# Kernel tuning notes

Measured on AMD Instinct MI355X. Metric: run time of the kernel, lower is better.

## Reference

```python
import jax, jax.numpy as jnp
import numpy as np

N = 4096      # num_nodes
D = 16        # intrinsic embed_dim (manifold points live in R^{D+1})
H = 64        # NCA hidden_dim
K_CURV = 1.0  # curvature K
SQRT_K = 1.0
TAU = 0.5     # temperature (distance decay)
K0 = 1.0      # coupling_strength
DT_PHASE = 0.1
DT_NCA = 0.1
EPS = 1e-7


def mdot(u, v):
    # Minkowski inner product <u,v>_L = -u0*v0 + sum_i ui*vi
    return jnp.sum(u[..., 1:] * v[..., 1:], axis=-1) - u[..., 0] * v[..., 0]


def proj_tangent(x, v):
    # project v onto tangent space at x: v + K<x,v>_L x
    return v + K_CURV * mdot(x, v)[..., None] * x


def exp_map(x, v):
    n = jnp.sqrt(jnp.clip(mdot(v, v), EPS))[..., None]
    return jnp.cosh(SQRT_K * n) * x + jnp.sinh(SQRT_K * n) / (SQRT_K * n) * v


def setup_inputs() -> dict:
    key = jax.random.key(0)
    ks = jax.random.split(key, 6)
    adjacency = jax.random.uniform(ks[0], (N, N), dtype=jnp.float32)
    # stable_initialization: tangent vector of radius 0.5, exp-mapped from origin
    v = jax.random.normal(ks[1], (N, D), dtype=jnp.float32)
    v = v * 0.5 / (jnp.linalg.norm(v, axis=-1, keepdims=True) + 1e-8)
    v_full = jnp.concatenate([jnp.zeros((N, 1), jnp.float32), v], axis=-1)
    origin = jnp.concatenate(
        [jnp.full((N, 1), 1.0 / SQRT_K, jnp.float32), jnp.zeros((N, D), jnp.float32)], axis=-1)
    h_states = exp_map(origin, proj_tangent(origin, v_full))
    # HAKORN Kuramoto parameters: per-node phases and natural frequencies
    theta = jax.random.uniform(ks[2], (N,), dtype=jnp.float32, minval=0.0, maxval=2.0 * np.pi)
    omega = jax.random.normal(ks[3], (N,), dtype=jnp.float32) * 0.1
    # NCA MLP weights (tangent-space update network)
    W1 = jax.random.normal(ks[4], (D + 1, H), jnp.float32) / np.sqrt(D + 1)
    b1 = jnp.zeros((H,), jnp.float32)
    W2 = jax.random.normal(ks[5], (H, D + 1), jnp.float32) / np.sqrt(H)
    b2 = jnp.zeros((D + 1,), jnp.float32)
    return {"adjacency": adjacency, "h_states": h_states, "theta": theta,
            "omega": omega, "W1": W1, "b1": b1, "W2": W2, "b2": b2, "num_steps": 2}


def _step(h, adjacency, theta, omega, W1, b1, W2, b2):
    X = h  # [N, D+1]
    # pairwise Minkowski gram G_ij = <x_i, x_j>_L  [N, N]
    G = X[:, 1:] @ X[:, 1:].T - jnp.outer(X[:, 0], X[:, 0])
    # hyperbolic distance matrix
    dmat = jnp.arccosh(jnp.clip(-K_CURV * G, 1.0)) / SQRT_K
    # distance-decayed adjacency coupling
    C = adjacency * jnp.exp(-dmat / TAU)
    # --- h_akorn: Kuramoto phase coupling (one Euler step), matvec form ---
    cs, sn = jnp.cos(theta), jnp.sin(theta)
    dtheta = omega + (K0 / N) * (cs * (C @ sn) - sn * (C @ cs))
    th = theta + DT_PHASE * dtheta
    cs2, sn2 = jnp.cos(th), jnp.sin(th)
    # phase-gated modulation weights [N, N]
    M = C * (0.5 * (1.0 + jnp.outer(cs2, cs2) + jnp.outer(sn2, sn2)))
    # synchronization order parameter r = |mean e^{i th}|
    r = jnp.sqrt(jnp.mean(cs2) ** 2 + jnp.mean(sn2) ** 2)
    # --- h_nca: weighted log-map aggregation + MLP + exp-map update ---
    # log_{x_i}(x_j) = alpha_ij * (x_j + K G_ij x_i),
    # alpha_ij = d_ij / ||x_j + K G_ij x_i||_L = d_ij / sqrt(K G_ij^2 - 1/K)
    unorm = jnp.sqrt(jnp.clip(K_CURV * G * G - 1.0 / K_CURV, EPS))
    alpha = jnp.where(dmat > 1e-6, dmat / unorm, 0.0)
    B = M * alpha  # [N, N]
    # m_i = sum_j B_ij x_j + K x_i sum_j B_ij G_ij  (avoids [N,N,D+1] tensor)
    m = B @ X + K_CURV * jnp.sum(B * G, axis=1, keepdims=True) * X
    v = jnp.tanh(m @ W1 + b1) @ W2 + b2
    v = proj_tangent(X, v)
    h_new = exp_map(X, DT_NCA * v)
    return h_new, M, r


def reference(adjacency, h_states, theta, omega, W1, b1, W2, b2, num_steps):
    h = h_states
    M = jnp.zeros_like(adjacency)
    r = jnp.asarray(0.0, h.dtype)
    for _ in range(num_steps):
        h, M, r = _step(h, adjacency, theta, omega, W1, b1, W2, b2)
    return h, M, r
```

## Files before the change

### kernel.cpp

```cpp
#include <hip/hip_runtime.h>
#include <math.h>

#define NN  4096
#define DP1 17
#define HID 64
#define EPSF 1e-7f

__device__ __forceinline__ float frcp(float x)  { return __builtin_amdgcn_rcpf(x); }
__device__ __forceinline__ float fsqrt(float x) { return __builtin_amdgcn_sqrtf(x); }
__device__ __forceinline__ float flogn(float x) { return __builtin_amdgcn_logf(x) * 0.69314718055994531f; }

__device__ __forceinline__ float uload(const float* __restrict__ p) {
    return __int_as_float(__builtin_amdgcn_readfirstlane(__float_as_int(*p)));
}

__device__ __forceinline__ float wred(float v) {
#pragma unroll
    for (int o = 32; o > 0; o >>= 1) v += __shfl_down(v, o, 64);
    return v;
}

__global__ __launch_bounds__(256) void initk(const float* __restrict__ h0,
                                             const float* __restrict__ theta,
                                             float* __restrict__ xt,
                                             float* __restrict__ snth,
                                             float* __restrict__ csth,
                                             float* __restrict__ racc) {
    int idx = blockIdx.x * 256 + threadIdx.x;
    if (idx < NN * DP1) {
        int i = idx / DP1, k = idx % DP1;
        xt[k * NN + i] = h0[idx];
    }
    if (idx < NN) {
        float t = theta[idx];
        snth[idx] = sinf(t);
        csth[idx] = cosf(t);
    }
    if (idx < 4) racc[idx] = 0.0f;
}

template <int R>
__global__ __launch_bounds__(256) void phaseA(const float* __restrict__ adj,
                                              const float* __restrict__ xrm,
                                              const float* __restrict__ xt,
                                              const float* __restrict__ snth,
                                              const float* __restrict__ csth,
                                              float* __restrict__ sumsn,
                                              float* __restrict__ sumcs) {
    const int tid = threadIdx.x;
    const int row0 = blockIdx.x * R;

    float xi[R][DP1];
#pragma unroll
    for (int r = 0; r < R; ++r)
#pragma unroll
        for (int k = 0; k < DP1; ++k) xi[r][k] = uload(xrm + (row0 + r) * DP1 + k);

    float accs[R], accc[R];
#pragma unroll
    for (int r = 0; r < R; ++r) { accs[r] = 0.f; accc[r] = 0.f; }

    for (int c = tid; c < NN; c += 256) {
        float xj[DP1];
#pragma unroll
        for (int k = 0; k < DP1; ++k) xj[k] = xt[k * NN + c];
        const float snj = snth[c], csj = csth[c];
#pragma unroll
        for (int r = 0; r < R; ++r) {
            float g = -xi[r][0] * xj[0];
#pragma unroll
            for (int k = 1; k < DP1; ++k) g = fmaf(xi[r][k], xj[k], g);
            const float a = fmaxf(-g, 1.0f);
            const float s = fsqrt(fmaxf(fmaf(a, a, -1.0f), 0.0f));
            const float t = a + s;
            const float e = frcp(t * t);
            const float Cij = adj[(row0 + r) * NN + c] * e;
            accs[r] = fmaf(Cij, snj, accs[r]);
            accc[r] = fmaf(Cij, csj, accc[r]);
        }
    }

    __shared__ float red[2 * R][4];
    const int wid = tid >> 6, lane = tid & 63;
#pragma unroll
    for (int r = 0; r < R; ++r) {
        float v1 = wred(accs[r]);
        float v2 = wred(accc[r]);
        if (lane == 0) { red[2 * r][wid] = v1; red[2 * r + 1][wid] = v2; }
    }
    __syncthreads();
    if (tid < 2 * R) {
        float s = red[tid][0] + red[tid][1] + red[tid][2] + red[tid][3];
        int r = tid >> 1;
        if (tid & 1) sumcs[row0 + r] = s;
        else         sumsn[row0 + r] = s;
    }
}

__global__ __launch_bounds__(256) void phaseB(const float* __restrict__ theta,
                                              const float* __restrict__ omega,
                                              const float* __restrict__ sumsn,
                                              const float* __restrict__ sumcs,
                                              float* __restrict__ cs2,
                                              float* __restrict__ sn2,
                                              float* __restrict__ racc) {
    const int i = blockIdx.x * 256 + threadIdx.x;
    const float th = theta[i];
    const float cs = cosf(th), sn = sinf(th);
    const float dth = omega[i] + (1.0f / (float)NN) * (cs * sumsn[i] - sn * sumcs[i]);
    const float t2 = th + 0.1f * dth;
    const float c2 = cosf(t2), s2 = sinf(t2);
    cs2[i] = c2;
    sn2[i] = s2;

    float sc = wred(c2);
    float ss = wred(s2);
    __shared__ float red[2][4];
    const int wid = threadIdx.x >> 6, lane = threadIdx.x & 63;
    if (lane == 0) { red[0][wid] = sc; red[1][wid] = ss; }
    __syncthreads();
    if (threadIdx.x == 0) {
        atomicAdd(racc,     red[0][0] + red[0][1] + red[0][2] + red[0][3]);
        atomicAdd(racc + 1, red[1][0] + red[1][1] + red[1][2] + red[1][3]);
    }
}

template <int R, bool WRITE_M>
__global__ __launch_bounds__(256) void phaseC(const float* __restrict__ adj,
                                              const float* __restrict__ xrm,
                                              const float* __restrict__ xt,
                                              const float* __restrict__ cs2,
                                              const float* __restrict__ sn2,
                                              float* __restrict__ mvec,
                                              float* __restrict__ s1v,
                                              float* __restrict__ Mout) {
    const int tid = threadIdx.x;
    const int row0 = blockIdx.x * R;

    float xi[R][DP1];
    float c2i[R], s2i[R];
#pragma unroll
    for (int r = 0; r < R; ++r) {
#pragma unroll
        for (int k = 0; k < DP1; ++k) xi[r][k] = uload(xrm + (row0 + r) * DP1 + k);
        c2i[r] = uload(cs2 + row0 + r);
        s2i[r] = uload(sn2 + row0 + r);
    }

    float accm[R][DP1], acc1[R];
#pragma unroll
    for (int r = 0; r < R; ++r) {
        acc1[r] = 0.f;
#pragma unroll
        for (int k = 0; k < DP1; ++k) accm[r][k] = 0.f;
    }

    for (int c = tid; c < NN; c += 256) {
        float xj[DP1];
#pragma unroll
        for (int k = 0; k < DP1; ++k) xj[k] = xt[k * NN + c];
        const float c2j = cs2[c], s2j = sn2[c];
#pragma unroll
        for (int r = 0; r < R; ++r) {
            float g = -xi[r][0] * xj[0];
#pragma unroll
            for (int k = 1; k < DP1; ++k) g = fmaf(xi[r][k], xj[k], g);
            const float a = fmaxf(-g, 1.0f);
            const float s = fsqrt(fmaxf(fmaf(a, a, -1.0f), 0.0f));
            const float t = a + s;
            const float e = frcp(t * t);
            const float Cij = adj[(row0 + r) * NN + c] * e;
            const float Mij = Cij * (0.5f * (1.0f + c2i[r] * c2j + s2i[r] * s2j));
            if (WRITE_M) Mout[(row0 + r) * NN + c] = Mij;
            const float dm = flogn(t);
            const float un = fsqrt(fmaxf(fmaf(g, g, -1.0f), EPSF));
            const float al = (dm > 1e-6f) ? (dm * frcp(un)) : 0.0f;
            const float Bij = Mij * al;
            acc1[r] = fmaf(Bij, g, acc1[r]);
#pragma unroll
            for (int k = 0; k < DP1; ++k) accm[r][k] = fmaf(Bij, xj[k], accm[r][k]);
        }
    }

    __shared__ float red[R * (DP1 + 1)][4];
    const int wid = tid >> 6, lane = tid & 63;
#pragma unroll
    for (int r = 0; r < R; ++r) {
#pragma unroll
        for (int k = 0; k < DP1; ++k) {
            float v = wred(accm[r][k]);
            if (lane == 0) red[r * (DP1 + 1) + k][wid] = v;
        }
        float v = wred(acc1[r]);
        if (lane == 0) red[r * (DP1 + 1) + DP1][wid] = v;
    }
    __syncthreads();
    if (tid < R * (DP1 + 1)) {
        float s = red[tid][0] + red[tid][1] + red[tid][2] + red[tid][3];
        int r = tid / (DP1 + 1), k = tid % (DP1 + 1);
        if (k < DP1) mvec[(row0 + r) * DP1 + k] = s;
        else         s1v[row0 + r] = s;
    }
}

__global__ __launch_bounds__(256) void phaseD(const float* __restrict__ xrm,
                                              const float* __restrict__ mvec,
                                              const float* __restrict__ s1v,
                                              const float* __restrict__ W1,
                                              const float* __restrict__ b1,
                                              const float* __restrict__ W2,
                                              const float* __restrict__ b2,
                                              float* __restrict__ xrm_out,
                                              float* __restrict__ xt_out,
                                              const float* __restrict__ racc,
                                              float* __restrict__ rout) {
    __shared__ float w1[DP1 * HID], w2[HID * DP1], bb1[HID], bb2[DP1];
    for (int j = threadIdx.x; j < DP1 * HID; j += 256) w1[j] = W1[j];
    for (int j = threadIdx.x; j < HID * DP1; j += 256) w2[j] = W2[j];
    if (threadIdx.x < HID) bb1[threadIdx.x] = b1[threadIdx.x];
    if (threadIdx.x < DP1) bb2[threadIdx.x] = b2[threadIdx.x];
    __syncthreads();

    const int i = blockIdx.x * 256 + threadIdx.x;

    float x[DP1], m[DP1];
    const float s1i = s1v[i];
#pragma unroll
    for (int k = 0; k < DP1; ++k) {
        x[k] = xrm[i * DP1 + k];
        m[k] = mvec[i * DP1 + k] + s1i * x[k];
    }

    float v[DP1];
#pragma unroll
    for (int k = 0; k < DP1; ++k) v[k] = bb2[k];
    for (int h = 0; h < HID; ++h) {
        float z = bb1[h];
#pragma unroll
        for (int k = 0; k < DP1; ++k) z = fmaf(m[k], w1[k * HID + h], z);
        const float zh = tanhf(z);
#pragma unroll
        for (int k = 0; k < DP1; ++k) v[k] = fmaf(zh, w2[h * DP1 + k], v[k]);
    }

    float md = -x[0] * v[0];
#pragma unroll
    for (int k = 1; k < DP1; ++k) md = fmaf(x[k], v[k], md);
#pragma unroll
    for (int k = 0; k < DP1; ++k) v[k] = fmaf(md, x[k], v[k]);

    float vd[DP1];
#pragma unroll
    for (int k = 0; k < DP1; ++k) vd[k] = 0.1f * v[k];
    float n2 = -vd[0] * vd[0];
#pragma unroll
    for (int k = 1; k < DP1; ++k) n2 = fmaf(vd[k], vd[k], n2);
    const float n = sqrtf(fmaxf(n2, EPSF));
    const float ch = coshf(n);
    const float sh = sinhf(n) / n;

    float hn[DP1];
#pragma unroll
    for (int k = 0; k < DP1; ++k) hn[k] = fmaf(ch, x[k], sh * vd[k]);

#pragma unroll
    for (int k = 0; k < DP1; ++k) xrm_out[i * DP1 + k] = hn[k];
    if (xt_out) {
#pragma unroll
        for (int k = 0; k < DP1; ++k) xt_out[k * NN + i] = hn[k];
    }
    if (rout && i == 0) {
        const float mc = racc[0] * (1.0f / (float)NN);
        const float ms = racc[1] * (1.0f / (float)NN);
        rout[0] = sqrtf(mc * mc + ms * ms);
    }
}

extern "C" void kernel_launch(void* const* d_in, const int* in_sizes, int n_in,
                              void* d_out, int out_size, void* d_ws, size_t ws_size,
                              hipStream_t stream) {
    const float* adj   = (const float*)d_in[0];
    const float* h0    = (const float*)d_in[1];
    const float* theta = (const float*)d_in[2];
    const float* omega = (const float*)d_in[3];
    const float* W1    = (const float*)d_in[4];
    const float* b1    = (const float*)d_in[5];
    const float* W2    = (const float*)d_in[6];
    const float* b2    = (const float*)d_in[7];

    float* out  = (float*)d_out;
    float* hout = out;
    float* Mout = out + NN * DP1;
    float* rout = Mout + (size_t)NN * NN;

    float* w     = (float*)d_ws;
    float* XT0   = w;
    float* XT1   = XT0 + NN * DP1;
    float* XRM1  = XT1 + NN * DP1;
    float* sumsn = XRM1 + NN * DP1;
    float* sumcs = sumsn + NN;
    float* cs2   = sumcs + NN;
    float* sn2   = cs2 + NN;
    float* snth  = sn2 + NN;
    float* csth  = snth + NN;
    float* mvec  = csth + NN;
    float* s1v   = mvec + NN * DP1;
    float* racc  = s1v + NN;

    constexpr int RA = 4;
    constexpr int RC = 4;

    initk<<<(NN * DP1 + 255) / 256, 256, 0, stream>>>(h0, theta, XT0, snth, csth, racc);

    phaseA<RA><<<NN / RA, 256, 0, stream>>>(adj, h0, XT0, snth, csth, sumsn, sumcs);
    phaseB<<<NN / 256, 256, 0, stream>>>(theta, omega, sumsn, sumcs, cs2, sn2, racc);
    phaseC<RC, false><<<NN / RC, 256, 0, stream>>>(adj, h0, XT0, cs2, sn2, mvec, s1v, nullptr);
    phaseD<<<NN / 256, 256, 0, stream>>>(h0, mvec, s1v, W1, b1, W2, b2,
                                         XRM1, XT1, nullptr, nullptr);

    phaseA<RA><<<NN / RA, 256, 0, stream>>>(adj, XRM1, XT1, snth, csth, sumsn, sumcs);
    phaseB<<<NN / 256, 256, 0, stream>>>(theta, omega, sumsn, sumcs, cs2, sn2, racc + 2);
    phaseC<RC, true><<<NN / RC, 256, 0, stream>>>(adj, XRM1, XT1, cs2, sn2, mvec, s1v, Mout);
    phaseD<<<NN / 256, 256, 0, stream>>>(XRM1, mvec, s1v, W1, b1, W2, b2,
                                         hout, nullptr, racc + 2, rout);
}
```

Measured before the change: 339.7 us.

## Switch to padded row-major node layout, one row per wave, and split columns

Replaces the transposed coordinate layout with a 20-float padded row-major layout read as five float4 loads per column. Each wave now owns one row, and the column range is split four ways across a second grid dimension, with partial sums written to workspace and reduced in the next phase. Sine and cosine are packed into float2, and launch bounds raise the occupancy targets. The intent is fewer register-heavy multi-row accumulators, vectorized loads and more blocks in flight, at the cost of extra partial-sum traffic and a wider per-thread gather stride.

```diff
diff --git a/kernel.cpp b/kernel.cpp
--- a/kernel.cpp
+++ b/kernel.cpp
@@ -1,10 +1,13 @@
 #include <hip/hip_runtime.h>
 #include <math.h>
 
-#define NN  4096
-#define DP1 17
-#define HID 64
+#define NN   4096
+#define DP1  17
+#define XPD  20
+#define HID  64
 #define EPSF 1e-7f
+#define CSPLIT 4
+#define COLS (NN / CSPLIT)
 
 __device__ __forceinline__ float frcp(float x)  { return __builtin_amdgcn_rcpf(x); }
 __device__ __forceinline__ float fsqrt(float x) { return __builtin_amdgcn_sqrtf(x); }
@@ -22,102 +25,94 @@
 
 __global__ __launch_bounds__(256) void initk(const float* __restrict__ h0,
                                              const float* __restrict__ theta,
-                                             float* __restrict__ xt,
-                                             float* __restrict__ snth,
-                                             float* __restrict__ csth,
+                                             float* __restrict__ xpad,
+                                             float2* __restrict__ scth,
                                              float* __restrict__ racc) {
-    int idx = blockIdx.x * 256 + threadIdx.x;
-    if (idx < NN * DP1) {
-        int i = idx / DP1, k = idx % DP1;
-        xt[k * NN + i] = h0[idx];
-    }
-    if (idx < NN) {
-        float t = theta[idx];
-        snth[idx] = sinf(t);
-        csth[idx] = cosf(t);
-    }
-    if (idx < 4) racc[idx] = 0.0f;
-}
-
-template <int R>
-__global__ __launch_bounds__(256) void phaseA(const float* __restrict__ adj,
-                                              const float* __restrict__ xrm,
-                                              const float* __restrict__ xt,
-                                              const float* __restrict__ snth,
-                                              const float* __restrict__ csth,
-                                              float* __restrict__ sumsn,
-                                              float* __restrict__ sumcs) {
-    const int tid = threadIdx.x;
-    const int row0 = blockIdx.x * R;
-
-    float xi[R][DP1];
-#pragma unroll
-    for (int r = 0; r < R; ++r)
-#pragma unroll
-        for (int k = 0; k < DP1; ++k) xi[r][k] = uload(xrm + (row0 + r) * DP1 + k);
-
-    float accs[R], accc[R];
-#pragma unroll
-    for (int r = 0; r < R; ++r) { accs[r] = 0.f; accc[r] = 0.f; }
-
-    for (int c = tid; c < NN; c += 256) {
-        float xj[DP1];
-#pragma unroll
-        for (int k = 0; k < DP1; ++k) xj[k] = xt[k * NN + c];
-        const float snj = snth[c], csj = csth[c];
-#pragma unroll
-        for (int r = 0; r < R; ++r) {
-            float g = -xi[r][0] * xj[0];
-#pragma unroll
-            for (int k = 1; k < DP1; ++k) g = fmaf(xi[r][k], xj[k], g);
-            const float a = fmaxf(-g, 1.0f);
-            const float s = fsqrt(fmaxf(fmaf(a, a, -1.0f), 0.0f));
-            const float t = a + s;
-            const float e = frcp(t * t);
-            const float Cij = adj[(row0 + r) * NN + c] * e;
-            accs[r] = fmaf(Cij, snj, accs[r]);
-            accc[r] = fmaf(Cij, csj, accc[r]);
-        }
-    }
-
-    __shared__ float red[2 * R][4];
-    const int wid = tid >> 6, lane = tid & 63;
-#pragma unroll
-    for (int r = 0; r < R; ++r) {
-        float v1 = wred(accs[r]);
-        float v2 = wred(accc[r]);
-        if (lane == 0) { red[2 * r][wid] = v1; red[2 * r + 1][wid] = v2; }
-    }
-    __syncthreads();
-    if (tid < 2 * R) {
-        float s = red[tid][0] + red[tid][1] + red[tid][2] + red[tid][3];
-        int r = tid >> 1;
-        if (tid & 1) sumcs[row0 + r] = s;
-        else         sumsn[row0 + r] = s;
-    }
-}
-
-__global__ __launch_bounds__(256) void phaseB(const float* __restrict__ theta,
-                                              const float* __restrict__ omega,
-                                              const float* __restrict__ sumsn,
-                                              const float* __restrict__ sumcs,
-                                              float* __restrict__ cs2,
-                                              float* __restrict__ sn2,
-                                              float* __restrict__ racc) {
     const int i = blockIdx.x * 256 + threadIdx.x;
+    if (i < NN) {
+#pragma unroll
+        for (int k = 0; k < DP1; ++k) xpad[i * XPD + k] = h0[i * DP1 + k];
+        xpad[i * XPD + 17] = 0.f; xpad[i * XPD + 18] = 0.f; xpad[i * XPD + 19] = 0.f;
+        const float t = theta[i];
+        scth[i] = make_float2(sinf(t), cosf(t));
+    }
+    if (i < 4) racc[i] = 0.0f;
+}
+
+#define GRAM(g, xi, q0, q1, q2, q3, q4)                                  \
+    do {                                                                 \
+        g = -xi[0] * q0.x;                                               \
+        g = fmaf(xi[1],  q0.y, g); g = fmaf(xi[2],  q0.z, g);            \
+        g = fmaf(xi[3],  q0.w, g); g = fmaf(xi[4],  q1.x, g);            \
+        g = fmaf(xi[5],  q1.y, g); g = fmaf(xi[6],  q1.z, g);            \
+        g = fmaf(xi[7],  q1.w, g); g = fmaf(xi[8],  q2.x, g);            \
+        g = fmaf(xi[9],  q2.y, g); g = fmaf(xi[10], q2.z, g);            \
+        g = fmaf(xi[11], q2.w, g); g = fmaf(xi[12], q3.x, g);            \
+        g = fmaf(xi[13], q3.y, g); g = fmaf(xi[14], q3.z, g);            \
+        g = fmaf(xi[15], q3.w, g); g = fmaf(xi[16], q4.x, g);            \
+    } while (0)
+
+__global__ __launch_bounds__(256, 8) void phaseA2(const float* __restrict__ adj,
+                                                  const float* __restrict__ xpad,
+                                                  const float2* __restrict__ scth,
+                                                  float* __restrict__ apart) {
+    const int lane = threadIdx.x & 63;
+    const int row  = blockIdx.x * 4 + (threadIdx.x >> 6);
+    const int c0   = blockIdx.y * COLS;
+
+    float xi[DP1];
+#pragma unroll
+    for (int k = 0; k < DP1; ++k) xi[k] = uload(xpad + row * XPD + k);
+
+    const float4* __restrict__ xp4 = (const float4*)xpad;
+    const float*  __restrict__ arow = adj + row * NN;
+
+    float accs = 0.f, accc = 0.f;
+    for (int c = c0 + lane; c < c0 + COLS; c += 64) {
+        const float4 q0 = xp4[c * 5 + 0], q1 = xp4[c * 5 + 1], q2 = xp4[c * 5 + 2],
+                     q3 = xp4[c * 5 + 3], q4 = xp4[c * 5 + 4];
+        float g; GRAM(g, xi, q0, q1, q2, q3, q4);
+        const float a = fmaxf(-g, 1.0f);
+        const float s = fsqrt(fmaxf(fmaf(a, a, -1.0f), 0.0f));
+        const float t = a + s;
+        const float e = frcp(t * t);
+        const float Cij = arow[c] * e;
+        const float2 sc = scth[c];
+        accs = fmaf(Cij, sc.x, accs);
+        accc = fmaf(Cij, sc.y, accc);
+    }
+    accs = wred(accs);
+    accc = wred(accc);
+    if (lane == 0) {
+        apart[(blockIdx.y * 2 + 0) * NN + row] = accs;
+        apart[(blockIdx.y * 2 + 1) * NN + row] = accc;
+    }
+}
+
+__global__ __launch_bounds__(256) void phaseB2(const float* __restrict__ theta,
+                                               const float* __restrict__ omega,
+                                               const float* __restrict__ apart,
+                                               float2* __restrict__ sc2,
+                                               float* __restrict__ racc) {
+    const int i = blockIdx.x * 256 + threadIdx.x;
+    float ss = 0.f, cc = 0.f;
+#pragma unroll
+    for (int s = 0; s < CSPLIT; ++s) {
+        ss += apart[(s * 2 + 0) * NN + i];
+        cc += apart[(s * 2 + 1) * NN + i];
+    }
     const float th = theta[i];
     const float cs = cosf(th), sn = sinf(th);
-    const float dth = omega[i] + (1.0f / (float)NN) * (cs * sumsn[i] - sn * sumcs[i]);
+    const float dth = omega[i] + (1.0f / (float)NN) * (cs * ss - sn * cc);
     const float t2 = th + 0.1f * dth;
     const float c2 = cosf(t2), s2 = sinf(t2);
-    cs2[i] = c2;
-    sn2[i] = s2;
-
-    float sc = wred(c2);
-    float ss = wred(s2);
+    sc2[i] = make_float2(c2, s2);
+
+    const float rc = wred(c2);
+    const float rs = wred(s2);
     __shared__ float red[2][4];
     const int wid = threadIdx.x >> 6, lane = threadIdx.x & 63;
-    if (lane == 0) { red[0][wid] = sc; red[1][wid] = ss; }
+    if (lane == 0) { red[0][wid] = rc; red[1][wid] = rs; }
     __syncthreads();
     if (threadIdx.x == 0) {
         atomicAdd(racc,     red[0][0] + red[0][1] + red[0][2] + red[0][3]);
@@ -125,95 +120,81 @@
     }
 }
 
-template <int R, bool WRITE_M>
-__global__ __launch_bounds__(256) void phaseC(const float* __restrict__ adj,
-                                              const float* __restrict__ xrm,
-                                              const float* __restrict__ xt,
-                                              const float* __restrict__ cs2,
-                                              const float* __restrict__ sn2,
-                                              float* __restrict__ mvec,
-                                              float* __restrict__ s1v,
-                                              float* __restrict__ Mout) {
-    const int tid = threadIdx.x;
-    const int row0 = blockIdx.x * R;
-
-    float xi[R][DP1];
-    float c2i[R], s2i[R];
-#pragma unroll
-    for (int r = 0; r < R; ++r) {
-#pragma unroll
-        for (int k = 0; k < DP1; ++k) xi[r][k] = uload(xrm + (row0 + r) * DP1 + k);
-        c2i[r] = uload(cs2 + row0 + r);
-        s2i[r] = uload(sn2 + row0 + r);
-    }
-
-    float accm[R][DP1], acc1[R];
-#pragma unroll
-    for (int r = 0; r < R; ++r) {
-        acc1[r] = 0.f;
-#pragma unroll
-        for (int k = 0; k < DP1; ++k) accm[r][k] = 0.f;
-    }
-
-    for (int c = tid; c < NN; c += 256) {
-        float xj[DP1];
-#pragma unroll
-        for (int k = 0; k < DP1; ++k) xj[k] = xt[k * NN + c];
-        const float c2j = cs2[c], s2j = sn2[c];
-#pragma unroll
-        for (int r = 0; r < R; ++r) {
-            float g = -xi[r][0] * xj[0];
-#pragma unroll
-            for (int k = 1; k < DP1; ++k) g = fmaf(xi[r][k], xj[k], g);
-            const float a = fmaxf(-g, 1.0f);
-            const float s = fsqrt(fmaxf(fmaf(a, a, -1.0f), 0.0f));
-            const float t = a + s;
-            const float e = frcp(t * t);
-            const float Cij = adj[(row0 + r) * NN + c] * e;
-            const float Mij = Cij * (0.5f * (1.0f + c2i[r] * c2j + s2i[r] * s2j));
-            if (WRITE_M) Mout[(row0 + r) * NN + c] = Mij;
-            const float dm = flogn(t);
-            const float un = fsqrt(fmaxf(fmaf(g, g, -1.0f), EPSF));
-            const float al = (dm > 1e-6f) ? (dm * frcp(un)) : 0.0f;
-            const float Bij = Mij * al;
-            acc1[r] = fmaf(Bij, g, acc1[r]);
-#pragma unroll
-            for (int k = 0; k < DP1; ++k) accm[r][k] = fmaf(Bij, xj[k], accm[r][k]);
-        }
-    }
-
-    __shared__ float red[R * (DP1 + 1)][4];
-    const int wid = tid >> 6, lane = tid & 63;
-#pragma unroll
-    for (int r = 0; r < R; ++r) {
-#pragma unroll
-        for (int k = 0; k < DP1; ++k) {
-            float v = wred(accm[r][k]);
-            if (lane == 0) red[r * (DP1 + 1) + k][wid] = v;
-        }
-        float v = wred(acc1[r]);
-        if (lane == 0) red[r * (DP1 + 1) + DP1][wid] = v;
-    }
-    __syncthreads();
-    if (tid < R * (DP1 + 1)) {
-        float s = red[tid][0] + red[tid][1] + red[tid][2] + red[tid][3];
-        int r = tid / (DP1 + 1), k = tid % (DP1 + 1);
-        if (k < DP1) mvec[(row0 + r) * DP1 + k] = s;
-        else         s1v[row0 + r] = s;
-    }
-}
-
-__global__ __launch_bounds__(256) void phaseD(const float* __restrict__ xrm,
-                                              const float* __restrict__ mvec,
-                                              const float* __restrict__ s1v,
-                                              const float* __restrict__ W1,
-                                              const float* __restrict__ b1,
-                                              const float* __restrict__ W2,
-                                              const float* __restrict__ b2,
-                                              float* __restrict__ xrm_out,
-                                              float* __restrict__ xt_out,
-                                              const float* __restrict__ racc,
-                                              float* __restrict__ rout) {
+template <bool WRITE_M>
+__global__ __launch_bounds__(256, 6) void phaseC2(const float* __restrict__ adj,
+                                                  const float* __restrict__ xpad,
+                                                  const float2* __restrict__ sc2,
+                                                  float* __restrict__ mpart,
+                                                  float* __restrict__ s1part,
+                                                  float* __restrict__ Mout) {
+    const int lane = threadIdx.x & 63;
+    const int row  = blockIdx.x * 4 + (threadIdx.x >> 6);
+    const int c0   = blockIdx.y * COLS;
+
+    float xi[DP1];
+#pragma unroll
+    for (int k = 0; k < DP1; ++k) xi[k] = uload(xpad + row * XPD + k);
+    const float c2i = uload(&((const float*)sc2)[row * 2 + 0]);
+    const float s2i = uload(&((const float*)sc2)[row * 2 + 1]);
+
+    const float4* __restrict__ xp4 = (const float4*)xpad;
+    const float*  __restrict__ arow = adj + row * NN;
+
+    float accm[DP1];
+#pragma unroll
+    for (int k = 0; k < DP1; ++k) accm[k] = 0.f;
+    float acc1 = 0.f;
+
+    for (int c = c0 + lane; c < c0 + COLS; c += 64) {
+        const float4 q0 = xp4[c * 5 + 0], q1 = xp4[c * 5 + 1], q2 = xp4[c * 5 + 2],
+                     q3 = xp4[c * 5 + 3], q4 = xp4[c * 5 + 4];
+        float g; GRAM(g, xi, q0, q1, q2, q3, q4);
+        const float a = fmaxf(-g, 1.0f);
+        const float s = fsqrt(fmaxf(fmaf(a, a, -1.0f), 0.0f));
+        const float t = a + s;
+        const float e = frcp(t * t);
+        const float Cij = arow[c] * e;
+        const float2 sc = sc2[c];
+        const float Mij = Cij * (0.5f * (1.0f + c2i * sc.x + s2i * sc.y));
+        if (WRITE_M) Mout[row * NN + c] = Mij;
+        const float dm = flogn(t);
+        const float un = fsqrt(fmaxf(fmaf(g, g, -1.0f), EPSF));
+        const float al = (dm > 1e-6f) ? (dm * frcp(un)) : 0.0f;
+        const float Bij = Mij * al;
+        acc1 = fmaf(Bij, g, acc1);
+        accm[0]  = fmaf(Bij, q0.x, accm[0]);  accm[1]  = fmaf(Bij, q0.y, accm[1]);
+        accm[2]  = fmaf(Bij, q0.z, accm[2]);  accm[3]  = fmaf(Bij, q0.w, accm[3]);
+        accm[4]  = fmaf(Bij, q1.x, accm[4]);  accm[5]  = fmaf(Bij, q1.y, accm[5]);
+        accm[6]  = fmaf(Bij, q1.z, accm[6]);  accm[7]  = fmaf(Bij, q1.w, accm[7]);
+        accm[8]  = fmaf(Bij, q2.x, accm[8]);  accm[9]  = fmaf(Bij, q2.y, accm[9]);
+        accm[10] = fmaf(Bij, q2.z, accm[10]); accm[11] = fmaf(Bij, q2.w, accm[11]);
+        accm[12] = fmaf(Bij, q3.x, accm[12]); accm[13] = fmaf(Bij, q3.y, accm[13]);
+        accm[14] = fmaf(Bij, q3.z, accm[14]); accm[15] = fmaf(Bij, q3.w, accm[15]);
+        accm[16] = fmaf(Bij, q4.x, accm[16]);
+    }
+
+#pragma unroll
+    for (int k = 0; k < DP1; ++k) accm[k] = wred(accm[k]);
+    acc1 = wred(acc1);
+    if (lane == 0) {
+#pragma unroll
+        for (int k = 0; k < DP1; ++k)
+            mpart[(blockIdx.y * NN + row) * DP1 + k] = accm[k];
+        s1part[blockIdx.y * NN + row] = acc1;
+    }
+}
+
+__global__ __launch_bounds__(256) void phaseD2(const float* __restrict__ xpad,
+                                               const float* __restrict__ mpart,
+                                               const float* __restrict__ s1part,
+                                               const float* __restrict__ W1,
+                                               const float* __restrict__ b1,
+                                               const float* __restrict__ W2,
+                                               const float* __restrict__ b2,
+                                               float* __restrict__ dense_out,
+                                               float* __restrict__ xpad_out,
+                                               const float* __restrict__ racc,
+                                               float* __restrict__ rout) {
     __shared__ float w1[DP1 * HID], w2[HID * DP1], bb1[HID], bb2[DP1];
     for (int j = threadIdx.x; j < DP1 * HID; j += 256) w1[j] = W1[j];
     for (int j = threadIdx.x; j < HID * DP1; j += 256) w2[j] = W2[j];
@@ -223,12 +204,21 @@
 
     const int i = blockIdx.x * 256 + threadIdx.x;
 
-    float x[DP1], m[DP1];
-    const float s1i = s1v[i];
+    float x[DP1];
+#pragma unroll
+    for (int k = 0; k < DP1; ++k) x[k] = xpad[i * XPD + k];
+
+    float s1 = 0.f;
+#pragma unroll
+    for (int s = 0; s < CSPLIT; ++s) s1 += s1part[s * NN + i];
+
+    float m[DP1];
 #pragma unroll
     for (int k = 0; k < DP1; ++k) {
-        x[k] = xrm[i * DP1 + k];
-        m[k] = mvec[i * DP1 + k] + s1i * x[k];
+        float mm = 0.f;
+#pragma unroll
+        for (int s = 0; s < CSPLIT; ++s) mm += mpart[(s * NN + i) * DP1 + k];
+        m[k] = mm + s1 * x[k];
     }
 
     float v[DP1];
@@ -263,11 +253,14 @@
 #pragma unroll
     for (int k = 0; k < DP1; ++k) hn[k] = fmaf(ch, x[k], sh * vd[k]);
 
-#pragma unroll
-    for (int k = 0; k < DP1; ++k) xrm_out[i * DP1 + k] = hn[k];
-    if (xt_out) {
-#pragma unroll
-        for (int k = 0; k < DP1; ++k) xt_out[k * NN + i] = hn[k];
+    if (dense_out) {
+#pragma unroll
+        for (int k = 0; k < DP1; ++k) dense_out[i * DP1 + k] = hn[k];
+    }
+    if (xpad_out) {
+#pragma unroll
+        for (int k = 0; k < DP1; ++k) xpad_out[i * XPD + k] = hn[k];
+        xpad_out[i * XPD + 17] = 0.f; xpad_out[i * XPD + 18] = 0.f; xpad_out[i * XPD + 19] = 0.f;
     }
     if (rout && i == 0) {
         const float mc = racc[0] * (1.0f / (float)NN);
@@ -293,34 +286,29 @@
     float* Mout = out + NN * DP1;
     float* rout = Mout + (size_t)NN * NN;
 
-    float* w     = (float*)d_ws;
-    float* XT0   = w;
-    float* XT1   = XT0 + NN * DP1;
-    float* XRM1  = XT1 + NN * DP1;
-    float* sumsn = XRM1 + NN * DP1;
-    float* sumcs = sumsn + NN;
-    float* cs2   = sumcs + NN;
-    float* sn2   = cs2 + NN;
-    float* snth  = sn2 + NN;
-    float* csth  = snth + NN;
-    float* mvec  = csth + NN;
-    float* s1v   = mvec + NN * DP1;
-    float* racc  = s1v + NN;
-
-    constexpr int RA = 4;
-    constexpr int RC = 4;
-
-    initk<<<(NN * DP1 + 255) / 256, 256, 0, stream>>>(h0, theta, XT0, snth, csth, racc);
-
-    phaseA<RA><<<NN / RA, 256, 0, stream>>>(adj, h0, XT0, snth, csth, sumsn, sumcs);
-    phaseB<<<NN / 256, 256, 0, stream>>>(theta, omega, sumsn, sumcs, cs2, sn2, racc);
-    phaseC<RC, false><<<NN / RC, 256, 0, stream>>>(adj, h0, XT0, cs2, sn2, mvec, s1v, nullptr);
-    phaseD<<<NN / 256, 256, 0, stream>>>(h0, mvec, s1v, W1, b1, W2, b2,
-                                         XRM1, XT1, nullptr, nullptr);
-
-    phaseA<RA><<<NN / RA, 256, 0, stream>>>(adj, XRM1, XT1, snth, csth, sumsn, sumcs);
-    phaseB<<<NN / 256, 256, 0, stream>>>(theta, omega, sumsn, sumcs, cs2, sn2, racc + 2);
-    phaseC<RC, true><<<NN / RC, 256, 0, stream>>>(adj, XRM1, XT1, cs2, sn2, mvec, s1v, Mout);
-    phaseD<<<NN / 256, 256, 0, stream>>>(XRM1, mvec, s1v, W1, b1, W2, b2,
-                                         hout, nullptr, racc + 2, rout);
-}
+    float* w      = (float*)d_ws;
+    float* xpad0  = w;
+    float* xpad1  = xpad0 + NN * XPD;
+    float2* scth  = (float2*)(xpad1 + NN * XPD);
+    float2* sc2   = scth + NN;
+    float* apart  = (float*)(sc2 + NN);
+    float* mpart  = apart + CSPLIT * 2 * NN;
+    float* s1part = mpart + CSPLIT * NN * DP1;
+    float* racc   = s1part + CSPLIT * NN;
+
+    const dim3 gAC(NN / 4, CSPLIT);
+
+    initk<<<NN / 256, 256, 0, stream>>>(h0, theta, xpad0, scth, racc);
+
+    phaseA2<<<gAC, 256, 0, stream>>>(adj, xpad0, scth, apart);
+    phaseB2<<<NN / 256, 256, 0, stream>>>(theta, omega, apart, sc2, racc);
+    phaseC2<false><<<gAC, 256, 0, stream>>>(adj, xpad0, sc2, mpart, s1part, nullptr);
+    phaseD2<<<NN / 256, 256, 0, stream>>>(xpad0, mpart, s1part, W1, b1, W2, b2,
+                                          nullptr, xpad1, nullptr, nullptr);
+
+    phaseA2<<<gAC, 256, 0, stream>>>(adj, xpad1, scth, apart);
+    phaseB2<<<NN / 256, 256, 0, stream>>>(theta, omega, apart, sc2, racc + 2);
+    phaseC2<true><<<gAC, 256, 0, stream>>>(adj, xpad1, sc2, mpart, s1part, Mout);
+    phaseD2<<<NN / 256, 256, 0, stream>>>(xpad1, mpart, s1part, W1, b1, W2, b2,
+                                          hout, nullptr, racc + 2, rout);
+}
```

After: 460.1 us. 1.35x slower.
